# Kernel tuning notes

Measured on AMD Instinct MI355X. Metric: run time of the kernel, lower is better.

The kernel has to match this reference:

```python
import jax, jax.numpy as jnp
import numpy as np

EPS = 1e-5

def _ln(x):
    # LayerNorm over last dim, no affine (elementwise_affine=False)
    mu = jnp.mean(x, axis=-1, keepdims=True)
    var = jnp.mean(jnp.square(x - mu), axis=-1, keepdims=True)
    return (x - mu) * jax.lax.rsqrt(var + EPS)

def setup_inputs() -> dict:
    key = jax.random.key(0)
    ks = jax.random.split(key, 6)
    B, L, D = 2, 2048, 2048
    s = 1.0 / np.sqrt(D)
    return {
        "x": jax.random.normal(ks[0], (B, L, D), jnp.float32),
        "Wq": jax.random.normal(ks[1], (D, D), jnp.float32) * s,
        "Wk": jax.random.normal(ks[2], (D, D), jnp.float32) * s,
        "Wv": jax.random.normal(ks[3], (D, D), jnp.float32) * s,
        "Wo": jax.random.normal(ks[4], (D, D), jnp.float32) * s,
        "bo": jnp.zeros((D,), jnp.float32),
    }

def reference(x, Wq, Wk, Wv, Wo, bo):
    B, L, D = x.shape
    H = 16
    hd = D // H
    q = (x @ Wq.T).reshape(B, L, H, hd)
    k = (x @ Wk.T).reshape(B, L, H, hd)
    v = (x @ Wv.T).reshape(B, L, H, hd)
    q = _ln(q)
    k = _ln(k)
    scores = jnp.einsum('blhd,bshd->bhls', q, k) / np.sqrt(hd)
    causal = jnp.tril(jnp.ones((L, L), bool))  # [L, L]
    scores = jnp.where(causal[None, None], scores, -jnp.inf)
    probs = jax.nn.softmax(scores, axis=-1)
    out = jnp.einsum('bhls,bshd->blhd', probs, v).reshape(B, L, D)
    return out @ Wo.T + bo
```

## Files before the change

### kernel.cpp

```cpp
#include <hip/hip_runtime.h>
#include <stdint.h>

typedef unsigned short u16;
typedef __attribute__((ext_vector_type(8))) unsigned short u16x8;
typedef __attribute__((ext_vector_type(8))) __bf16 bf16x8;
typedef __attribute__((ext_vector_type(4))) float f32x4;
typedef __attribute__((ext_vector_type(8))) float f32x8;

#define AS_G __attribute__((address_space(1)))
#define AS_L __attribute__((address_space(3)))

static __device__ __forceinline__ void gload_lds16(const u16* g, u16* l) {
  __builtin_amdgcn_global_load_lds((AS_G void*)(u16*)g, (AS_L void*)l, 16, 0, 0);
}

static __device__ __forceinline__ u16 f2bf(float f) {
  union { float f; unsigned u; } v; v.f = f;
  return (u16)((v.u + 0x7FFFu + ((v.u >> 16) & 1u)) >> 16);
}
static __device__ __forceinline__ float bf2f(u16 b) {
  union { unsigned u; float f; } v; v.u = ((unsigned)b) << 16;
  return v.f;
}
static __device__ __forceinline__ u16 f2bf_trunc(float f) {
  union { float f; unsigned u; } v; v.f = f;
  return (u16)(v.u >> 16);
}

#define BAR() do { asm volatile("" ::: "memory"); __builtin_amdgcn_s_barrier(); asm volatile("" ::: "memory"); } while (0)

__global__ __launch_bounds__(256) void cast_all(
    const float* __restrict__ x, const float* __restrict__ Wq,
    const float* __restrict__ Wk, const float* __restrict__ Wv,
    const float* __restrict__ Wo,
    u16* __restrict__ xb, u16* __restrict__ Wcat, u16* __restrict__ Wob)
{
  const int NX = (4096 * 2048) / 8;
  const int NW = (2048 * 2048) / 8;
  const int total = NX + 4 * NW;
  for (int i = blockIdx.x * 256 + threadIdx.x; i < total; i += gridDim.x * 256) {
    const float* src; u16* dst; int idx;
    if (i < NX)               { src = x;  dst = xb;                 idx = i; }
    else if (i < NX + NW)     { src = Wq; dst = Wcat;               idx = i - NX; }
    else if (i < NX + 2*NW)   { src = Wk; dst = Wcat + 2048*2048;   idx = i - NX - NW; }
    else if (i < NX + 3*NW)   { src = Wv; dst = Wcat + 2*2048*2048; idx = i - NX - 2*NW; }
    else                      { src = Wo; dst = Wob;                idx = i - NX - 3*NW; }
    f32x8 v = *(const f32x8*)(src + (size_t)idx * 8);
    u16x8 o;
    #pragma unroll
    for (int e = 0; e < 8; e++) o[e] = f2bf(v[e]);
    *(u16x8*)(dst + (size_t)idx * 8) = o;
  }
}

#define MFMA2(q, x00, x01, x10, x11) \
  do { __builtin_amdgcn_s_setprio(1); \
    _Pragma("unroll") \
    for (int nf = 0; nf < 3; ++nf) { \
      acc[2*(q)][nf]   = __builtin_amdgcn_mfma_f32_16x16x32_bf16(x00, breg[nf][0], acc[2*(q)][nf], 0, 0, 0); \
      acc[2*(q)][nf]   = __builtin_amdgcn_mfma_f32_16x16x32_bf16(x01, breg[nf][1], acc[2*(q)][nf], 0, 0, 0); \
      acc[2*(q)+1][nf] = __builtin_amdgcn_mfma_f32_16x16x32_bf16(x10, breg[nf][0], acc[2*(q)+1][nf], 0, 0, 0); \
      acc[2*(q)+1][nf] = __builtin_amdgcn_mfma_f32_16x16x32_bf16(x11, breg[nf][1], acc[2*(q)+1][nf], 0, 0, 0); \
    } \
    __builtin_amdgcn_s_setprio(0); } while (0)

__global__ __launch_bounds__(512, 2) void gemm256(
    const u16* __restrict__ A, const u16* __restrict__ B,
    u16* __restrict__ Cout, int M, int N, int K)
{
  __shared__ u16 As[2][256 * 64];
  __shared__ u16 Bs[2][192 * 64];
  const int tid = threadIdx.x, lane = tid & 63, wid = tid >> 6;
  const int wm = wid >> 2, wn = wid & 3;

  const int nbx = gridDim.x;
  const int nwg = gridDim.x * gridDim.y;
  const int flat = blockIdx.y * nbx + blockIdx.x;
  const int swz = (flat & 7) * (nwg >> 3) + (flat >> 3);
  const int row0 = (swz / nbx) * 256, col0 = (swz % nbx) * 192;
  const int NT = K >> 6;

  const int sr  = tid >> 3;
  const int scb = ((tid & 7) * 16) ^ ((sr & 7) << 4);

  auto stA = [&](int buf, int t, int u) {
    const u16* src = A + (size_t)(row0 + u * 64 + sr) * K + t * 64 + (scb >> 1);
    gload_lds16(src, As[buf] + u * 4096 + wid * 512);
  };
  auto stB = [&](int buf, int t, int u) {
    const u16* src = B + (size_t)(col0 + u * 64 + sr) * K + t * 64 + (scb >> 1);
    gload_lds16(src, Bs[buf] + u * 4096 + wid * 512);
  };
  auto ldA = [&](int buf, int mf, int k) {
    int ra = wm * 128 + mf * 16 + (lane & 15);
    int bc = (k * 64 + ((lane >> 4) << 4)) ^ ((ra & 7) << 4);
    return *(const bf16x8*)((const char*)As[buf] + ra * 128 + bc);
  };
  auto ldB = [&](int buf, int nf, int k) {
    int rb = wn * 48 + nf * 16 + (lane & 15);
    int bc = (k * 64 + ((lane >> 4) << 4)) ^ ((rb & 7) << 4);
    return *(const bf16x8*)((const char*)Bs[buf] + rb * 128 + bc);
  };

  f32x4 acc[8][3] = {};
  bf16x8 breg[3][2];

  stA(0, 0, 0); stA(0, 0, 1); stA(0, 0, 2); stA(0, 0, 3);
  stB(0, 0, 0); stB(0, 0, 1); stB(0, 0, 2);
  stB(1, 1, 0); stB(1, 1, 1); stB(1, 1, 2);
  asm volatile("s_waitcnt vmcnt(3)" ::: "memory");
  BAR();

  for (int it = 0; it < NT / 2; ++it) {
    const int t1  = 2 * it + 1;
    const int pf0 = (2 * it + 2 < NT) ? (2 * it + 2) : (NT - 1);
    const int pf1 = (2 * it + 3 < NT) ? (2 * it + 3) : (NT - 1);
    #pragma unroll
    for (int hf = 0; hf < 2; ++hf) {
      const int cb = hf;
      #pragma unroll
      for (int nf = 0; nf < 3; ++nf) {
        breg[nf][0] = ldB(cb, nf, 0);
        breg[nf][1] = ldB(cb, nf, 1);
      }
      bf16x8 a00 = ldA(cb, 0, 0), a01 = ldA(cb, 0, 1);
      bf16x8 a10 = ldA(cb, 1, 0), a11 = ldA(cb, 1, 1);
      BAR();
      if (hf == 0) { stA(1, t1, 0); stA(1, t1, 1); } else { stA(0, pf0, 0); stA(0, pf0, 1); }
      MFMA2(0, a00, a01, a10, a11);
      a00 = ldA(cb, 2, 0); a01 = ldA(cb, 2, 1);
      a10 = ldA(cb, 3, 0); a11 = ldA(cb, 3, 1);
      BAR();
      if (hf == 0) { stA(1, t1, 2); stA(1, t1, 3); } else { stA(0, pf0, 2); stA(0, pf0, 3); }
      MFMA2(1, a00, a01, a10, a11);
      a00 = ldA(cb, 4, 0); a01 = ldA(cb, 4, 1);
      a10 = ldA(cb, 5, 0); a11 = ldA(cb, 5, 1);
      BAR();
      if (hf == 0) { stB(0, pf0, 0); stB(0, pf0, 1); } else { stB(1, pf1, 0); stB(1, pf1, 1); }
      MFMA2(2, a00, a01, a10, a11);
      a00 = ldA(cb, 6, 0); a01 = ldA(cb, 6, 1);
      a10 = ldA(cb, 7, 0); a11 = ldA(cb, 7, 1);
      BAR();
      if (hf == 0) stB(0, pf0, 2); else stB(1, pf1, 2);
      MFMA2(3, a00, a01, a10, a11);
      asm volatile("s_waitcnt vmcnt(3)" ::: "memory");
      BAR();
    }
  }
  asm volatile("s_waitcnt vmcnt(0)" ::: "memory");

  #pragma unroll
  for (int mf = 0; mf < 8; ++mf) {
    #pragma unroll
    for (int nf = 0; nf < 3; ++nf) {
      #pragma unroll
      for (int e = 0; e < 4; ++e) {
        int r = row0 + wm * 128 + mf * 16 + (lane >> 4) * 4 + e;
        int c = col0 + wn * 48 + nf * 16 + (lane & 15);
        Cout[(size_t)r * N + c] = f2bf(acc[mf][nf][e]);
      }
    }
  }
}

template<bool FP32OUT>
__global__ __launch_bounds__(256) void gemm_nt(
    const u16* __restrict__ A, const u16* __restrict__ B,
    void* __restrict__ Cout, const float* __restrict__ bias,
    int M, int N, int K)
{
  __shared__ u16 As[128 * 32];
  __shared__ u16 Bs[128 * 32];
  const int tid = threadIdx.x;
  const int lane = tid & 63;
  const int wid = tid >> 6;
  const int wr = wid >> 1, wc = wid & 1;
  const int row0 = blockIdx.y * 128, col0 = blockIdx.x * 128;

  const u16* Ag = A + (size_t)(row0 + (tid >> 2)) * K + (tid & 3) * 8;
  const u16* Bg = B + (size_t)(col0 + (tid >> 2)) * K + (tid & 3) * 8;
  u16* AsW0 = As + wid * 512;
  u16* AsW1 = As + 2048 + wid * 512;
  u16* BsW0 = Bs + wid * 512;
  u16* BsW1 = Bs + 2048 + wid * 512;

  f32x4 acc[4][4] = {};

  for (int k0 = 0; k0 < K; k0 += 32) {
    gload_lds16(Ag + k0, AsW0);
    gload_lds16(Ag + (size_t)64 * K + k0, AsW1);
    gload_lds16(Bg + k0, BsW0);
    gload_lds16(Bg + (size_t)64 * K + k0, BsW1);
    __syncthreads();
    bf16x8 a[4], b[4];
    #pragma unroll
    for (int mt = 0; mt < 4; mt++)
      a[mt] = *(const bf16x8*)(As + (wr*64 + mt*16 + (lane & 15)) * 32 + (lane >> 4) * 8);
    #pragma unroll
    for (int nt = 0; nt < 4; nt++)
      b[nt] = *(const bf16x8*)(Bs + (wc*64 + nt*16 + (lane & 15)) * 32 + (lane >> 4) * 8);
    #pragma unroll
    for (int mt = 0; mt < 4; mt++)
      #pragma unroll
      for (int nt = 0; nt < 4; nt++)
        acc[mt][nt] = __builtin_amdgcn_mfma_f32_16x16x32_bf16(a[mt], b[nt], acc[mt][nt], 0, 0, 0);
    __syncthreads();
  }

  #pragma unroll
  for (int mt = 0; mt < 4; mt++) {
    #pragma unroll
    for (int nt = 0; nt < 4; nt++) {
      #pragma unroll
      for (int e = 0; e < 4; e++) {
        int r = row0 + wr*64 + mt*16 + (lane >> 4) * 4 + e;
        int c = col0 + wc*64 + nt*16 + (lane & 15);
        if constexpr (FP32OUT) {
          ((float*)Cout)[(size_t)r * N + c] = acc[mt][nt][e] + bias[c];
        } else {
          ((u16*)Cout)[(size_t)r * N + c] = f2bf(acc[mt][nt][e]);
        }
      }
    }
  }
}

__global__ __launch_bounds__(256) void ln_qk(u16* __restrict__ QKV)
{
  const float SC2 = 0.08838834764831845f * 1.4426950408889634f;
  const int row = blockIdx.x;
  const int t = threadIdx.x;
  const int h = t >> 4;
  const int e0 = (t & 15) * 8;
  u16* rowp = QKV + (size_t)row * 6144;
  #pragma unroll
  for (int part = 0; part < 2; part++) {
    u16* p = rowp + part * 2048 + h * 128 + e0;
    u16x8 raw = *(const u16x8*)p;
    float v[8]; float s = 0.f, s2 = 0.f;
    #pragma unroll
    for (int e = 0; e < 8; e++) { v[e] = bf2f(raw[e]); s += v[e]; s2 += v[e]*v[e]; }
    #pragma unroll
    for (int m = 1; m < 16; m <<= 1) { s += __shfl_xor(s, m); s2 += __shfl_xor(s2, m); }
    float mu = s * (1.f / 128.f);
    float var = s2 * (1.f / 128.f) - mu * mu;
    float rstd = rsqrtf(var + 1e-5f) * (part == 0 ? SC2 : 1.0f);
    u16x8 o;
    #pragma unroll
    for (int e = 0; e < 8; e++) o[e] = f2bf((v[e] - mu) * rstd);
    *(u16x8*)p = o;
  }
}

__global__ __launch_bounds__(256) void transpose_v(const u16* __restrict__ QKV, u16* __restrict__ Vt)
{
  __shared__ u16 T[64 * 65];
  const int d0 = blockIdx.x * 64;
  const int l0 = blockIdx.y * 64;
  const int bh = blockIdx.z;
  const int b = bh >> 4, h = bh & 15;
  const int t = threadIdx.x;
  #pragma unroll
  for (int i = 0; i < 2; i++) {
    int c = t + i * 256;
    int l = c >> 3, dc = (c & 7) * 8;
    u16x8 v = *(const u16x8*)(QKV + (size_t)(b*2048 + l0 + l) * 6144 + 4096 + h*128 + d0 + dc);
    #pragma unroll
    for (int e = 0; e < 8; e++) T[l * 65 + dc + e] = v[e];
  }
  __syncthreads();
  #pragma unroll
  for (int i = 0; i < 2; i++) {
    int c = t + i * 256;
    int d = c >> 3, lc = (c & 7) * 8;
    u16x8 o;
    #pragma unroll
    for (int e = 0; e < 8; e++) o[e] = T[(lc + e) * 65 + d];
    *(u16x8*)(Vt + (size_t)((b*16 + h) * 128 + d0 + d) * 2048 + l0 + lc) = o;
  }
}

static __device__ __forceinline__ void stage_k_tile(
    const u16* __restrict__ QKV, int b, int h, int j0, u16* Kbuf, int tid, int wid)
{
  #pragma unroll
  for (int i = 0; i < 4; i++) {
    int c = i * 256 + tid;
    int r = c >> 4, ob = (c & 15) * 16;
    int cb = ob ^ ((r & 7) << 4);
    const u16* g = QKV + (size_t)(b*2048 + j0 + r) * 6144 + 2048 + h*128 + (cb >> 1);
    gload_lds16(g, Kbuf + (i * 256 + wid * 64) * 8);
  }
}
static __device__ __forceinline__ void stage_v_tile(
    const u16* __restrict__ Vt, int b, int h, int j0, u16* Vbuf, int tid, int wid)
{
  #pragma unroll
  for (int i = 0; i < 4; i++) {
    int c = i * 256 + tid;
    int r = c >> 3, ob = (c & 7) * 16;
    int cb = ob ^ ((r & 7) << 4);
    const u16* g = Vt + (size_t)((b*16 + h) * 128 + r) * 2048 + j0 + (cb >> 1);
    gload_lds16(g, Vbuf + (i * 256 + wid * 64) * 8);
  }
}

__global__ __launch_bounds__(256) void attn(
    const u16* __restrict__ QKV, const u16* __restrict__ Vt, u16* __restrict__ AO)
{
  const int flat = blockIdx.x + (blockIdx.y << 4) + (blockIdx.z << 8);
  const int swz = (flat & 7) * 64 + (flat >> 3);
  const int pair = swz & 15;
  const int h = (swz >> 4) & 15;
  const int b = swz >> 8;
  const int tid = threadIdx.x, lane = tid & 63, wid = tid >> 6;

  __shared__ u16 Ks[2][64 * 128];
  __shared__ u16 Vs[2][128 * 64];
  __shared__ u16 Ps[4][16 * 64];

  for (int side = 0; side < 2; side++) {
    const int pp = side ? (31 - pair) : pair;
    const int l0 = pp * 64;
    const int ntile = pp + 1;

    bf16x8 qa[4];
    const u16* qrow = QKV + (size_t)(b*2048 + l0 + wid*16 + (lane & 15)) * 6144
                      + h*128 + (lane >> 4) * 8;
    #pragma unroll
    for (int ks = 0; ks < 4; ks++) qa[ks] = *(const bf16x8*)(qrow + ks * 32);

    f32x4 o[8] = {};
    float mrun[4] = {-1e30f, -1e30f, -1e30f, -1e30f};
    float lrun[4] = {};

    stage_v_tile(Vt, b, h, 0, Vs[0], tid, wid);
    stage_k_tile(QKV, b, h, 0, Ks[0], tid, wid);
    int cur = 0;

    for (int t = 0; t < ntile; t++) {
      if (t + 1 < ntile) {
        stage_v_tile(Vt, b, h, (t + 1) * 64, Vs[cur ^ 1], tid, wid);
        stage_k_tile(QKV, b, h, (t + 1) * 64, Ks[cur ^ 1], tid, wid);
        asm volatile("s_waitcnt vmcnt(8)" ::: "memory");
      } else {
        asm volatile("s_waitcnt vmcnt(0)" ::: "memory");
      }
      __builtin_amdgcn_s_barrier();
      asm volatile("" ::: "memory");

      f32x4 s[4] = {};
      const char* Kc = (const char*)Ks[cur];
      __builtin_amdgcn_s_setprio(1);
      #pragma unroll
      for (int nt = 0; nt < 4; nt++) {
        #pragma unroll
        for (int ks = 0; ks < 4; ks++) {
          int r = nt * 16 + (lane & 15);
          int cb = ks * 64 + (lane >> 4) * 16;
          bf16x8 kb = *(const bf16x8*)(Kc + r * 256 + (cb ^ ((lane & 7) << 4)));
          s[nt] = __builtin_amdgcn_mfma_f32_16x16x32_bf16(qa[ks], kb, s[nt], 0, 0, 0);
        }
      }
      __builtin_amdgcn_s_setprio(0);

      if (t == ntile - 1) {
        #pragma unroll
        for (int nt = 0; nt < 4; nt++) {
          #pragma unroll
          for (int e = 0; e < 4; e++) {
            int i_loc = wid * 16 + (lane >> 4) * 4 + e;
            int j_loc = nt * 16 + (lane & 15);
            if (j_loc > i_loc) s[nt][e] = -1e30f;
          }
        }
      }

      float pmax[4];
      #pragma unroll
      for (int e = 0; e < 4; e++) {
        float v = fmaxf(fmaxf(s[0][e], s[1][e]), fmaxf(s[2][e], s[3][e]));
        v = fmaxf(v, __shfl_xor(v, 1));
        v = fmaxf(v, __shfl_xor(v, 2));
        v = fmaxf(v, __shfl_xor(v, 4));
        v = fmaxf(v, __shfl_xor(v, 8));
        pmax[e] = v;
      }
      bool need = (pmax[0] > mrun[0] + 8.f) || (pmax[1] > mrun[1] + 8.f) ||
                  (pmax[2] > mrun[2] + 8.f) || (pmax[3] > mrun[3] + 8.f);
      if (__any(need)) {
        float alpha[4];
        #pragma unroll
        for (int e = 0; e < 4; e++) {
          float mi = fmaxf(mrun[e], pmax[e]);
          alpha[e] = exp2f(mrun[e] - mi);
          mrun[e] = mi;
          lrun[e] *= alpha[e];
        }
        #pragma unroll
        for (int dt = 0; dt < 8; dt++)
          #pragma unroll
          for (int e = 0; e < 4; e++)
            o[dt][e] *= alpha[e];
      }

      char* PsW = (char*)Ps[wid];
      #pragma unroll
      for (int nt = 0; nt < 4; nt++) {
        #pragma unroll
        for (int e = 0; e < 4; e++) {
          float p = exp2f(s[nt][e] - mrun[e]);
          lrun[e] += p;
          int i_ = (lane >> 4) * 4 + e;
          int jb = (nt * 16 + (lane & 15)) * 2;
          *(u16*)(PsW + i_ * 128 + (jb ^ ((i_ & 7) << 4))) = f2bf_trunc(p);
        }
      }

      const char* Vc = (const char*)Vs[cur];
      __builtin_amdgcn_s_setprio(1);
      #pragma unroll
      for (int ks = 0; ks < 2; ks++) {
        int ir = lane & 15;
        int jb = ks * 64 + (lane >> 4) * 16;
        bf16x8 pa = *(const bf16x8*)(PsW + ir * 128 + (jb ^ ((ir & 7) << 4)));
        #pragma unroll
        for (int dt = 0; dt < 8; dt++) {
          int dr = dt * 16 + (lane & 15);
          bf16x8 vb = *(const bf16x8*)(Vc + dr * 128 + (jb ^ ((lane & 7) << 4)));
          o[dt] = __builtin_amdgcn_mfma_f32_16x16x32_bf16(pa, vb, o[dt], 0, 0, 0);
        }
      }
      __builtin_amdgcn_s_setprio(0);

      asm volatile("s_waitcnt lgkmcnt(0)" ::: "memory");
      __builtin_amdgcn_s_barrier();
      asm volatile("" ::: "memory");
      cur ^= 1;
    }

    #pragma unroll
    for (int e = 0; e < 4; e++) {
      float l = lrun[e];
      l += __shfl_xor(l, 1);
      l += __shfl_xor(l, 2);
      l += __shfl_xor(l, 4);
      l += __shfl_xor(l, 8);
      float inv = 1.0f / l;
      int rglob = b * 2048 + l0 + wid * 16 + (lane >> 4) * 4 + e;
      #pragma unroll
      for (int dt = 0; dt < 8; dt++)
        AO[(size_t)rglob * 2048 + h * 128 + dt * 16 + (lane & 15)] = f2bf(o[dt][e] * inv);
    }
  }
}

extern "C" void kernel_launch(void* const* d_in, const int* in_sizes, int n_in,
                              void* d_out, int out_size, void* d_ws, size_t ws_size,
                              hipStream_t stream)
{
  const float* x  = (const float*)d_in[0];
  const float* Wq = (const float*)d_in[1];
  const float* Wk = (const float*)d_in[2];
  const float* Wv = (const float*)d_in[3];
  const float* Wo = (const float*)d_in[4];
  const float* bo = (const float*)d_in[5];

  char* ws = (char*)d_ws;
  u16* xb   = (u16*)(ws);
  u16* Wcat = (u16*)(ws + 16777216);
  u16* Wob  = (u16*)(ws + 16777216 + 25165824);
  u16* QKV  = (u16*)(ws + 16777216 + 25165824 + 8388608);
  u16* AO   = xb;
  u16* Vt   = Wcat;

  cast_all<<<dim3(2048), dim3(256), 0, stream>>>(x, Wq, Wk, Wv, Wo, xb, Wcat, Wob);
  gemm256<<<dim3(32, 16), dim3(512), 0, stream>>>(xb, Wcat, QKV, 4096, 6144, 2048);
  ln_qk<<<dim3(4096), dim3(256), 0, stream>>>(QKV);
  transpose_v<<<dim3(2, 32, 32), dim3(256), 0, stream>>>(QKV, Vt);
  attn<<<dim3(16, 16, 2), dim3(256), 0, stream>>>(QKV, Vt, AO);
  gemm_nt<true><<<dim3(16, 32), dim3(256), 0, stream>>>(AO, Wob, d_out, bo, 4096, 2048, 2048);
}
```

Before: 295.1 us.

## Fuse QK layernorm into QKV GEMM epilogue and pipeline output projection GEMM

The QKV GEMM tile widens from 256x192 to 256x256 so that each wave pair covers whole 128-wide heads. Per-head LayerNorm and the softmax scale for Q and K are then computed in the epilogue through an LDS reduction, which removes the separate ln_qk pass over QKV. The simple output-projection GEMM is replaced by a double-buffered 256x128 kernel with LDS swizzling and direct-to-LDS loads. The trade-offs are dropping the block swizzle (worse L2 locality), higher register pressure from the 8x4 accumulator, and a 384-block grid with uneven wave balance.

```diff
diff --git a/kernel.cpp b/kernel.cpp
--- a/kernel.cpp
+++ b/kernel.cpp
@@ -56,7 +56,7 @@
 #define MFMA2(q, x00, x01, x10, x11) \
   do { __builtin_amdgcn_s_setprio(1); \
     _Pragma("unroll") \
-    for (int nf = 0; nf < 3; ++nf) { \
+    for (int nf = 0; nf < 4; ++nf) { \
       acc[2*(q)][nf]   = __builtin_amdgcn_mfma_f32_16x16x32_bf16(x00, breg[nf][0], acc[2*(q)][nf], 0, 0, 0); \
       acc[2*(q)][nf]   = __builtin_amdgcn_mfma_f32_16x16x32_bf16(x01, breg[nf][1], acc[2*(q)][nf], 0, 0, 0); \
       acc[2*(q)+1][nf] = __builtin_amdgcn_mfma_f32_16x16x32_bf16(x10, breg[nf][0], acc[2*(q)+1][nf], 0, 0, 0); \
@@ -69,27 +69,26 @@
     u16* __restrict__ Cout, int M, int N, int K)
 {
   __shared__ u16 As[2][256 * 64];
-  __shared__ u16 Bs[2][192 * 64];
+  __shared__ u16 Bs[2][256 * 64];
   const int tid = threadIdx.x, lane = tid & 63, wid = tid >> 6;
   const int wm = wid >> 2, wn = wid & 3;
-
-  const int nbx = gridDim.x;
-  const int nwg = gridDim.x * gridDim.y;
-  const int flat = blockIdx.y * nbx + blockIdx.x;
-  const int swz = (flat & 7) * (nwg >> 3) + (flat >> 3);
-  const int row0 = (swz / nbx) * 256, col0 = (swz % nbx) * 192;
+  const int row0 = blockIdx.y * 256, col0 = blockIdx.x * 256;
   const int NT = K >> 6;
 
   const int sr  = tid >> 3;
   const int scb = ((tid & 7) * 16) ^ ((sr & 7) << 4);
 
-  auto stA = [&](int buf, int t, int u) {
-    const u16* src = A + (size_t)(row0 + u * 64 + sr) * K + t * 64 + (scb >> 1);
-    gload_lds16(src, As[buf] + u * 4096 + wid * 512);
-  };
-  auto stB = [&](int buf, int t, int u) {
-    const u16* src = B + (size_t)(col0 + u * 64 + sr) * K + t * 64 + (scb >> 1);
-    gload_lds16(src, Bs[buf] + u * 4096 + wid * 512);
+  auto stA = [&](int buf, int t, int half) {
+    const u16* src = A + (size_t)(row0 + half * 128 + sr) * K + t * 64 + (scb >> 1);
+    u16* dst = As[buf] + half * 8192 + wid * 512;
+    gload_lds16(src, dst);
+    gload_lds16(src + (size_t)64 * K, dst + 4096);
+  };
+  auto stB = [&](int buf, int t, int half) {
+    const u16* src = B + (size_t)(col0 + half * 128 + sr) * K + t * 64 + (scb >> 1);
+    u16* dst = Bs[buf] + half * 8192 + wid * 512;
+    gload_lds16(src, dst);
+    gload_lds16(src + (size_t)64 * K, dst + 4096);
   };
   auto ldA = [&](int buf, int mf, int k) {
     int ra = wm * 128 + mf * 16 + (lane & 15);
@@ -97,18 +96,17 @@
     return *(const bf16x8*)((const char*)As[buf] + ra * 128 + bc);
   };
   auto ldB = [&](int buf, int nf, int k) {
-    int rb = wn * 48 + nf * 16 + (lane & 15);
+    int rb = wn * 64 + nf * 16 + (lane & 15);
     int bc = (k * 64 + ((lane >> 4) << 4)) ^ ((rb & 7) << 4);
     return *(const bf16x8*)((const char*)Bs[buf] + rb * 128 + bc);
   };
 
-  f32x4 acc[8][3] = {};
-  bf16x8 breg[3][2];
-
-  stA(0, 0, 0); stA(0, 0, 1); stA(0, 0, 2); stA(0, 0, 3);
-  stB(0, 0, 0); stB(0, 0, 1); stB(0, 0, 2);
-  stB(1, 1, 0); stB(1, 1, 1); stB(1, 1, 2);
-  asm volatile("s_waitcnt vmcnt(3)" ::: "memory");
+  f32x4 acc[8][4] = {};
+  bf16x8 breg[4][2];
+
+  stA(0, 0, 0); stA(0, 0, 1); stB(0, 0, 0); stB(0, 0, 1);
+  stB(1, 1, 0); stB(1, 1, 1);
+  asm volatile("s_waitcnt vmcnt(4)" ::: "memory");
   BAR();
 
   for (int it = 0; it < NT / 2; ++it) {
@@ -119,136 +117,193 @@
     for (int hf = 0; hf < 2; ++hf) {
       const int cb = hf;
       #pragma unroll
-      for (int nf = 0; nf < 3; ++nf) {
+      for (int nf = 0; nf < 4; ++nf) {
         breg[nf][0] = ldB(cb, nf, 0);
         breg[nf][1] = ldB(cb, nf, 1);
       }
       bf16x8 a00 = ldA(cb, 0, 0), a01 = ldA(cb, 0, 1);
       bf16x8 a10 = ldA(cb, 1, 0), a11 = ldA(cb, 1, 1);
       BAR();
-      if (hf == 0) { stA(1, t1, 0); stA(1, t1, 1); } else { stA(0, pf0, 0); stA(0, pf0, 1); }
+      if (hf == 0) stA(1, t1, 0); else stA(0, pf0, 0);
       MFMA2(0, a00, a01, a10, a11);
       a00 = ldA(cb, 2, 0); a01 = ldA(cb, 2, 1);
       a10 = ldA(cb, 3, 0); a11 = ldA(cb, 3, 1);
       BAR();
-      if (hf == 0) { stA(1, t1, 2); stA(1, t1, 3); } else { stA(0, pf0, 2); stA(0, pf0, 3); }
+      if (hf == 0) stA(1, t1, 1); else stA(0, pf0, 1);
       MFMA2(1, a00, a01, a10, a11);
       a00 = ldA(cb, 4, 0); a01 = ldA(cb, 4, 1);
       a10 = ldA(cb, 5, 0); a11 = ldA(cb, 5, 1);
       BAR();
-      if (hf == 0) { stB(0, pf0, 0); stB(0, pf0, 1); } else { stB(1, pf1, 0); stB(1, pf1, 1); }
+      if (hf == 0) stB(0, pf0, 0); else stB(1, pf1, 0);
       MFMA2(2, a00, a01, a10, a11);
       a00 = ldA(cb, 6, 0); a01 = ldA(cb, 6, 1);
       a10 = ldA(cb, 7, 0); a11 = ldA(cb, 7, 1);
       BAR();
-      if (hf == 0) stB(0, pf0, 2); else stB(1, pf1, 2);
+      if (hf == 0) stB(0, pf0, 1); else stB(1, pf1, 1);
       MFMA2(3, a00, a01, a10, a11);
-      asm volatile("s_waitcnt vmcnt(3)" ::: "memory");
+      asm volatile("s_waitcnt vmcnt(4)" ::: "memory");
       BAR();
     }
   }
   asm volatile("s_waitcnt vmcnt(0)" ::: "memory");
+  BAR();
+
+  if (col0 < 4096) {
+    float* red = (float*)As;
+    #pragma unroll
+    for (int mf = 0; mf < 8; ++mf) {
+      #pragma unroll
+      for (int e = 0; e < 4; ++e) {
+        float s = acc[mf][0][e] + acc[mf][1][e] + acc[mf][2][e] + acc[mf][3][e];
+        float q = acc[mf][0][e]*acc[mf][0][e] + acc[mf][1][e]*acc[mf][1][e]
+                + acc[mf][2][e]*acc[mf][2][e] + acc[mf][3][e]*acc[mf][3][e];
+        #pragma unroll
+        for (int m = 1; m < 16; m <<= 1) { s += __shfl_xor(s, m); q += __shfl_xor(q, m); }
+        if ((lane & 15) == 0) {
+          int rl = mf * 16 + (lane >> 4) * 4 + e;
+          red[wid * 256 + rl * 2]     = s;
+          red[wid * 256 + rl * 2 + 1] = q;
+        }
+      }
+    }
+    BAR();
+    const float mul = (col0 < 2048) ? (0.08838834764831845f * 1.4426950408889634f) : 1.0f;
+    #pragma unroll
+    for (int mf = 0; mf < 8; ++mf) {
+      #pragma unroll
+      for (int e = 0; e < 4; ++e) {
+        int rl = mf * 16 + (lane >> 4) * 4 + e;
+        float s = red[wid * 256 + rl * 2]     + red[(wid ^ 1) * 256 + rl * 2];
+        float q = red[wid * 256 + rl * 2 + 1] + red[(wid ^ 1) * 256 + rl * 2 + 1];
+        float mu = s * (1.f / 128.f);
+        float var = q * (1.f / 128.f) - mu * mu;
+        float rstd = rsqrtf(var + 1e-5f) * mul;
+        int r = row0 + wm * 128 + rl;
+        #pragma unroll
+        for (int nf = 0; nf < 4; ++nf) {
+          int c = col0 + wn * 64 + nf * 16 + (lane & 15);
+          Cout[(size_t)r * N + c] = f2bf((acc[mf][nf][e] - mu) * rstd);
+        }
+      }
+    }
+  } else {
+    #pragma unroll
+    for (int mf = 0; mf < 8; ++mf) {
+      #pragma unroll
+      for (int nf = 0; nf < 4; ++nf) {
+        #pragma unroll
+        for (int e = 0; e < 4; ++e) {
+          int r = row0 + wm * 128 + mf * 16 + (lane >> 4) * 4 + e;
+          int c = col0 + wn * 64 + nf * 16 + (lane & 15);
+          Cout[(size_t)r * N + c] = f2bf(acc[mf][nf][e]);
+        }
+      }
+    }
+  }
+}
+
+__global__ __launch_bounds__(512, 2) void gemm_ao(
+    const u16* __restrict__ A, const u16* __restrict__ B,
+    float* __restrict__ C, const float* __restrict__ bias,
+    int M, int N, int K)
+{
+  __shared__ u16 As[2][256 * 64];
+  __shared__ u16 Bs[2][128 * 64];
+  const int tid = threadIdx.x, lane = tid & 63, wid = tid >> 6;
+  const int wm = wid >> 1, wn = wid & 1;
+  const int row0 = blockIdx.y * 256, col0 = blockIdx.x * 128;
+  const int NT = K >> 6;
+
+  const int sr  = tid >> 3;
+  const int scb = ((tid & 7) * 16) ^ ((sr & 7) << 4);
+
+  auto stA = [&](int buf, int t, int u) {
+    const u16* src = A + (size_t)(row0 + u * 64 + sr) * K + t * 64 + (scb >> 1);
+    gload_lds16(src, As[buf] + u * 4096 + wid * 512);
+  };
+  auto stB = [&](int buf, int t, int u) {
+    const u16* src = B + (size_t)(col0 + u * 64 + sr) * K + t * 64 + (scb >> 1);
+    gload_lds16(src, Bs[buf] + u * 4096 + wid * 512);
+  };
+  auto ldA = [&](int buf, int mf, int k) {
+    int ra = wm * 64 + mf * 16 + (lane & 15);
+    int bc = (k * 64 + ((lane >> 4) << 4)) ^ ((ra & 7) << 4);
+    return *(const bf16x8*)((const char*)As[buf] + ra * 128 + bc);
+  };
+  auto ldB = [&](int buf, int nf, int k) {
+    int rb = wn * 64 + nf * 16 + (lane & 15);
+    int bc = (k * 64 + ((lane >> 4) << 4)) ^ ((rb & 7) << 4);
+    return *(const bf16x8*)((const char*)Bs[buf] + rb * 128 + bc);
+  };
+
+  f32x4 acc[4][4] = {};
+  bf16x8 breg[4][2];
+
+  stA(0, 0, 0); stA(0, 0, 1); stA(0, 0, 2); stA(0, 0, 3);
+  stB(0, 0, 0); stB(0, 0, 1);
+  stB(1, 1, 0); stB(1, 1, 1);
+  asm volatile("s_waitcnt vmcnt(2)" ::: "memory");
+  BAR();
+
+  for (int it = 0; it < NT / 2; ++it) {
+    const int t1  = 2 * it + 1;
+    const int pf0 = (2 * it + 2 < NT) ? (2 * it + 2) : (NT - 1);
+    const int pf1 = (2 * it + 3 < NT) ? (2 * it + 3) : (NT - 1);
+    #pragma unroll
+    for (int hf = 0; hf < 2; ++hf) {
+      const int cb = hf;
+      #pragma unroll
+      for (int nf = 0; nf < 4; ++nf) { breg[nf][0] = ldB(cb, nf, 0); breg[nf][1] = ldB(cb, nf, 1); }
+      bf16x8 a0 = ldA(cb, 0, 0), a1 = ldA(cb, 0, 1);
+      BAR();
+      if (hf == 0) { stA(1, t1, 0); stA(1, t1, 1); } else { stA(0, pf0, 0); stA(0, pf0, 1); }
+      __builtin_amdgcn_s_setprio(1);
+      #pragma unroll
+      for (int nf = 0; nf < 4; ++nf) {
+        acc[0][nf] = __builtin_amdgcn_mfma_f32_16x16x32_bf16(a0, breg[nf][0], acc[0][nf], 0, 0, 0);
+        acc[0][nf] = __builtin_amdgcn_mfma_f32_16x16x32_bf16(a1, breg[nf][1], acc[0][nf], 0, 0, 0);
+      }
+      __builtin_amdgcn_s_setprio(0);
+      bf16x8 b0 = ldA(cb, 1, 0), b1 = ldA(cb, 1, 1);
+      bf16x8 c0 = ldA(cb, 2, 0), c1 = ldA(cb, 2, 1);
+      BAR();
+      if (hf == 0) { stA(1, t1, 2); stA(1, t1, 3); } else { stA(0, pf0, 2); stA(0, pf0, 3); }
+      __builtin_amdgcn_s_setprio(1);
+      #pragma unroll
+      for (int nf = 0; nf < 4; ++nf) {
+        acc[1][nf] = __builtin_amdgcn_mfma_f32_16x16x32_bf16(b0, breg[nf][0], acc[1][nf], 0, 0, 0);
+        acc[1][nf] = __builtin_amdgcn_mfma_f32_16x16x32_bf16(b1, breg[nf][1], acc[1][nf], 0, 0, 0);
+        acc[2][nf] = __builtin_amdgcn_mfma_f32_16x16x32_bf16(c0, breg[nf][0], acc[2][nf], 0, 0, 0);
+        acc[2][nf] = __builtin_amdgcn_mfma_f32_16x16x32_bf16(c1, breg[nf][1], acc[2][nf], 0, 0, 0);
+      }
+      __builtin_amdgcn_s_setprio(0);
+      a0 = ldA(cb, 3, 0); a1 = ldA(cb, 3, 1);
+      BAR();
+      if (hf == 0) { stB(0, pf0, 0); stB(0, pf0, 1); } else { stB(1, pf1, 0); stB(1, pf1, 1); }
+      __builtin_amdgcn_s_setprio(1);
+      #pragma unroll
+      for (int nf = 0; nf < 4; ++nf) {
+        acc[3][nf] = __builtin_amdgcn_mfma_f32_16x16x32_bf16(a0, breg[nf][0], acc[3][nf], 0, 0, 0);
+        acc[3][nf] = __builtin_amdgcn_mfma_f32_16x16x32_bf16(a1, breg[nf][1], acc[3][nf], 0, 0, 0);
+      }
+      __builtin_amdgcn_s_setprio(0);
+      asm volatile("s_waitcnt vmcnt(2)" ::: "memory");
+      BAR();
+    }
+  }
+  asm volatile("s_waitcnt vmcnt(0)" ::: "memory");
 
   #pragma unroll
-  for (int mf = 0; mf < 8; ++mf) {
-    #pragma unroll
-    for (int nf = 0; nf < 3; ++nf) {
+  for (int mf = 0; mf < 4; ++mf) {
+    #pragma unroll
+    for (int nf = 0; nf < 4; ++nf) {
       #pragma unroll
       for (int e = 0; e < 4; ++e) {
-        int r = row0 + wm * 128 + mf * 16 + (lane >> 4) * 4 + e;
-        int c = col0 + wn * 48 + nf * 16 + (lane & 15);
-        Cout[(size_t)r * N + c] = f2bf(acc[mf][nf][e]);
-      }
-    }
-  }
-}
-
-template<bool FP32OUT>
-__global__ __launch_bounds__(256) void gemm_nt(
-    const u16* __restrict__ A, const u16* __restrict__ B,
-    void* __restrict__ Cout, const float* __restrict__ bias,
-    int M, int N, int K)
-{
-  __shared__ u16 As[128 * 32];
-  __shared__ u16 Bs[128 * 32];
-  const int tid = threadIdx.x;
-  const int lane = tid & 63;
-  const int wid = tid >> 6;
-  const int wr = wid >> 1, wc = wid & 1;
-  const int row0 = blockIdx.y * 128, col0 = blockIdx.x * 128;
-
-  const u16* Ag = A + (size_t)(row0 + (tid >> 2)) * K + (tid & 3) * 8;
-  const u16* Bg = B + (size_t)(col0 + (tid >> 2)) * K + (tid & 3) * 8;
-  u16* AsW0 = As + wid * 512;
-  u16* AsW1 = As + 2048 + wid * 512;
-  u16* BsW0 = Bs + wid * 512;
-  u16* BsW1 = Bs + 2048 + wid * 512;
-
-  f32x4 acc[4][4] = {};
-
-  for (int k0 = 0; k0 < K; k0 += 32) {
-    gload_lds16(Ag + k0, AsW0);
-    gload_lds16(Ag + (size_t)64 * K + k0, AsW1);
-    gload_lds16(Bg + k0, BsW0);
-    gload_lds16(Bg + (size_t)64 * K + k0, BsW1);
-    __syncthreads();
-    bf16x8 a[4], b[4];
-    #pragma unroll
-    for (int mt = 0; mt < 4; mt++)
-      a[mt] = *(const bf16x8*)(As + (wr*64 + mt*16 + (lane & 15)) * 32 + (lane >> 4) * 8);
-    #pragma unroll
-    for (int nt = 0; nt < 4; nt++)
-      b[nt] = *(const bf16x8*)(Bs + (wc*64 + nt*16 + (lane & 15)) * 32 + (lane >> 4) * 8);
-    #pragma unroll
-    for (int mt = 0; mt < 4; mt++)
-      #pragma unroll
-      for (int nt = 0; nt < 4; nt++)
-        acc[mt][nt] = __builtin_amdgcn_mfma_f32_16x16x32_bf16(a[mt], b[nt], acc[mt][nt], 0, 0, 0);
-    __syncthreads();
-  }
-
-  #pragma unroll
-  for (int mt = 0; mt < 4; mt++) {
-    #pragma unroll
-    for (int nt = 0; nt < 4; nt++) {
-      #pragma unroll
-      for (int e = 0; e < 4; e++) {
-        int r = row0 + wr*64 + mt*16 + (lane >> 4) * 4 + e;
-        int c = col0 + wc*64 + nt*16 + (lane & 15);
-        if constexpr (FP32OUT) {
-          ((float*)Cout)[(size_t)r * N + c] = acc[mt][nt][e] + bias[c];
-        } else {
-          ((u16*)Cout)[(size_t)r * N + c] = f2bf(acc[mt][nt][e]);
-        }
-      }
-    }
-  }
-}
-
-__global__ __launch_bounds__(256) void ln_qk(u16* __restrict__ QKV)
-{
-  const float SC2 = 0.08838834764831845f * 1.4426950408889634f;
-  const int row = blockIdx.x;
-  const int t = threadIdx.x;
-  const int h = t >> 4;
-  const int e0 = (t & 15) * 8;
-  u16* rowp = QKV + (size_t)row * 6144;
-  #pragma unroll
-  for (int part = 0; part < 2; part++) {
-    u16* p = rowp + part * 2048 + h * 128 + e0;
-    u16x8 raw = *(const u16x8*)p;
-    float v[8]; float s = 0.f, s2 = 0.f;
-    #pragma unroll
-    for (int e = 0; e < 8; e++) { v[e] = bf2f(raw[e]); s += v[e]; s2 += v[e]*v[e]; }
-    #pragma unroll
-    for (int m = 1; m < 16; m <<= 1) { s += __shfl_xor(s, m); s2 += __shfl_xor(s2, m); }
-    float mu = s * (1.f / 128.f);
-    float var = s2 * (1.f / 128.f) - mu * mu;
-    float rstd = rsqrtf(var + 1e-5f) * (part == 0 ? SC2 : 1.0f);
-    u16x8 o;
-    #pragma unroll
-    for (int e = 0; e < 8; e++) o[e] = f2bf((v[e] - mu) * rstd);
-    *(u16x8*)p = o;
+        int r = row0 + wm * 64 + mf * 16 + (lane >> 4) * 4 + e;
+        int c = col0 + wn * 64 + nf * 16 + (lane & 15);
+        C[(size_t)r * N + c] = acc[mf][nf][e] + bias[c];
+      }
+    }
   }
 }
 
@@ -475,9 +530,8 @@
   u16* Vt   = Wcat;
 
   cast_all<<<dim3(2048), dim3(256), 0, stream>>>(x, Wq, Wk, Wv, Wo, xb, Wcat, Wob);
-  gemm256<<<dim3(32, 16), dim3(512), 0, stream>>>(xb, Wcat, QKV, 4096, 6144, 2048);
-  ln_qk<<<dim3(4096), dim3(256), 0, stream>>>(QKV);
+  gemm256<<<dim3(24, 16), dim3(512), 0, stream>>>(xb, Wcat, QKV, 4096, 6144, 2048);
   transpose_v<<<dim3(2, 32, 32), dim3(256), 0, stream>>>(QKV, Vt);
   attn<<<dim3(16, 16, 2), dim3(256), 0, stream>>>(QKV, Vt, AO);
-  gemm_nt<true><<<dim3(16, 32), dim3(256), 0, stream>>>(AO, Wob, d_out, bo, 4096, 2048, 2048);
-}
+  gemm_ao<<<dim3(16, 16), dim3(512), 0, stream>>>(AO, Wob, (float*)d_out, bo, 4096, 2048, 2048);
+}
```

New measurement: 279.9 us. 5.2% less time.
